# Performance work log

Measured on AMD Instinct MI355X. Metric: run time of the kernel, lower is better.

Reference implementation:

```python
import itertools
import jax, jax.numpy as jnp
import numpy as np

B, RES, RES_, STRIDE = 512, 14, 7, 2
IN_DIM, OUT_DIM, KEY_DIM, H, ATTN_RATIO = 256, 512, 16, 8, 2
NH_KD = KEY_DIM * H          # 128
D = ATTN_RATIO * KEY_DIM     # 32
DH = D * H                   # 256
KV_OUT = DH + NH_KD          # 384
N, N_ = RES * RES, RES_ * RES_   # 196, 49
EPS = 1e-5
SCALE = KEY_DIM ** -0.5


def _build_bias_idxs():
    points = list(itertools.product(range(RES), range(RES)))
    points_ = list(itertools.product(range(RES_), range(RES_)))
    offsets, idxs = {}, []
    for p1 in points_:
        for p2 in points:
            off = (abs(p1[0] * STRIDE - p2[0]), abs(p1[1] * STRIDE - p2[1]))
            if off not in offsets:
                offsets[off] = len(offsets)
            idxs.append(offsets[off])
    return np.array(idxs, dtype=np.int32).reshape(N_, N), len(offsets)


def _bn(x, g, b, m, v):
    # inference-mode BatchNorm1d over last dim
    return (x - m) * (g * jax.lax.rsqrt(v + EPS)) + b


def _hardswish(x):
    return x * jnp.clip(x + 3.0, 0.0, 6.0) * (1.0 / 6.0)


def setup_inputs() -> dict:
    key = jax.random.key(0)
    ks = jax.random.split(key, 16)
    idxs_np, n_off = _build_bias_idxs()
    inp = {
        "x": jax.random.normal(ks[0], (B, N, IN_DIM), jnp.float32),
        "w_kv": jax.random.normal(ks[1], (KV_OUT, IN_DIM), jnp.float32) * 0.02,
        "kv_g": jnp.ones((KV_OUT,), jnp.float32),
        "kv_b": jax.random.normal(ks[2], (KV_OUT,), jnp.float32) * 0.01,
        "kv_m": jax.random.normal(ks[3], (KV_OUT,), jnp.float32) * 0.01,
        "kv_v": jax.random.uniform(ks[4], (KV_OUT,), jnp.float32) + 0.5,
        "w_q": jax.random.normal(ks[5], (NH_KD, IN_DIM), jnp.float32) * 0.02,
        "q_g": jnp.ones((NH_KD,), jnp.float32),
        "q_b": jax.random.normal(ks[6], (NH_KD,), jnp.float32) * 0.01,
        "q_m": jax.random.normal(ks[7], (NH_KD,), jnp.float32) * 0.01,
        "q_v": jax.random.uniform(ks[8], (NH_KD,), jnp.float32) + 0.5,
        "w_p": jax.random.normal(ks[9], (OUT_DIM, DH), jnp.float32) * 0.02,
        "p_g": jnp.ones((OUT_DIM,), jnp.float32),
        "p_b": jax.random.normal(ks[10], (OUT_DIM,), jnp.float32) * 0.01,
        "p_m": jax.random.normal(ks[11], (OUT_DIM,), jnp.float32) * 0.01,
        "p_v": jax.random.uniform(ks[12], (OUT_DIM,), jnp.float32) + 0.5,
        "ab_table": jax.random.normal(ks[13], (H, n_off), jnp.float32) * 0.02,
        "bias_idxs": jnp.asarray(idxs_np),  # [N_, N] int32
    }
    return inp


def reference(x, w_kv, kv_g, kv_b, kv_m, kv_v,
              w_q, q_g, q_b, q_m, q_v,
              w_p, p_g, p_b, p_m, p_v,
              ab_table, bias_idxs):
    Bx = x.shape[0]
    # kv projection: [B, N, KV_OUT] -> split heads into k [B,H,N,KEY_DIM], v [B,H,N,D]
    kv = _bn(jnp.einsum('bnc,oc->bno', x, w_kv), kv_g, kv_b, kv_m, kv_v)
    kv = kv.reshape(Bx, N, H, KEY_DIM + D)
    k = kv[..., :KEY_DIM].transpose(0, 2, 1, 3)   # [B,H,N,KEY_DIM]
    v = kv[..., KEY_DIM:].transpose(0, 2, 1, 3)   # [B,H,N,D]
    # query path: spatial subsample then Linear+BN
    xs = x.reshape(Bx, RES, RES, IN_DIM)[:, ::STRIDE, ::STRIDE].reshape(Bx, N_, IN_DIM)
    q = _bn(jnp.einsum('bnc,oc->bno', xs, w_q), q_g, q_b, q_m, q_v)
    q = q.reshape(Bx, N_, H, KEY_DIM).transpose(0, 2, 1, 3)  # [B,H,N_,KEY_DIM]
    # relative-position bias gather: [H, N_, N]
    ab = ab_table[:, bias_idxs]
    attn = jnp.einsum('bhqd,bhkd->bhqk', q, k) * SCALE + ab
    attn = jax.nn.softmax(attn, axis=-1)
    out = jnp.einsum('bhqk,bhkd->bhqd', attn, v)           # [B,H,N_,D]
    out = out.transpose(0, 2, 1, 3).reshape(Bx, N_, DH)
    out = _hardswish(out)
    out = _bn(jnp.einsum('bnd,od->bno', out, w_p), p_g, p_b, p_m, p_v)
    return out
```

## Files before the change

### kernel.cpp

```cpp
#include <hip/hip_runtime.h>

typedef __attribute__((ext_vector_type(8))) short bf16x8;
typedef __attribute__((ext_vector_type(4))) float f32x4;
typedef __attribute__((ext_vector_type(4))) short short4v;
typedef __attribute__((ext_vector_type(4))) unsigned int u32x4;
typedef __attribute__((ext_vector_type(2))) unsigned int u32x2;

#define DEVFN static __device__ __forceinline__

DEVFN short f2bf(float f) {
  unsigned int u = __builtin_bit_cast(unsigned int, f);
  unsigned int r = (u + 0x7FFFu + ((u >> 16) & 1u)) >> 16;
  return (short)r;
}

DEVFN unsigned int pack2bf(float a, float b) {
  unsigned int lo = (unsigned int)(unsigned short)f2bf(a);
  unsigned int hi = (unsigned int)(unsigned short)f2bf(b);
  return lo | (hi << 16);
}

DEVFN f32x4 mfma_bf16(bf16x8 a, bf16x8 b, f32x4 c) {
  return __builtin_amdgcn_mfma_f32_16x16x32_bf16(a, b, c, 0, 0, 0);
}

DEVFN f32x4 zero4() { f32x4 z = {0.f, 0.f, 0.f, 0.f}; return z; }
DEVFN bf16x8 zero8() { bf16x8 z = {0,0,0,0,0,0,0,0}; return z; }

DEVFN void gload_lds16(const void* g, void* l) {
  __builtin_amdgcn_global_load_lds(
      (const __attribute__((address_space(1))) unsigned int*)g,
      (__attribute__((address_space(3))) unsigned int*)l, 16, 0, 0);
}

DEVFN bf16x8 lds8(const short* p) {
  short4v lo = *reinterpret_cast<const short4v*>(p);
  short4v hi = *reinterpret_cast<const short4v*>(p + 4);
  bf16x8 r;
  r[0] = lo[0]; r[1] = lo[1]; r[2] = lo[2]; r[3] = lo[3];
  r[4] = hi[0]; r[5] = hi[1]; r[6] = hi[2]; r[7] = hi[3];
  return r;
}

DEVFN bf16x8 cvt8v(float4 u0, float4 u1) {
  bf16x8 r;
  r[0] = f2bf(u0.x); r[1] = f2bf(u0.y); r[2] = f2bf(u0.z); r[3] = f2bf(u0.w);
  r[4] = f2bf(u1.x); r[5] = f2bf(u1.y); r[6] = f2bf(u1.z); r[7] = f2bf(u1.w);
  return r;
}

DEVFN float bfhi2f(unsigned int hi16) {
  return __builtin_bit_cast(float, hi16 << 16);
}
DEVFN float bfhi2f_hi(unsigned int word) {
  return __builtin_bit_cast(float, word & 0xffff0000u);
}

__global__ void pack_w_k(const float* __restrict__ w, const float* __restrict__ g,
                         const float* __restrict__ b, const float* __restrict__ m,
                         const float* __restrict__ v, short* __restrict__ pk,
                         float* __restrict__ bias, int O) {
  const int t = blockIdx.x * 256 + threadIdx.x;
  const int nt = O >> 4;
  const int total = nt * 8 * 64;
  if (t < total) {
    int lane = t & 63;
    int j = (t >> 6) % nt;
    int c = (t >> 6) / nt;
    int row = j * 16 + (lane & 15);
    int col = c * 32 + (lane >> 4) * 8;
    float s = g[row] * rsqrtf(v[row] + 1e-5f);
    const float* wp = w + (size_t)row * 256 + col;
    short* o = pk + (size_t)t * 8;
#pragma unroll
    for (int e = 0; e < 8; ++e) o[e] = f2bf(wp[e] * s);
  }
  if (t < O) {
    float s = g[t] * rsqrtf(v[t] + 1e-5f);
    bias[t] = b[t] - m[t] * s;
  }
}

__global__ void ab_gather2(const float* __restrict__ tab,
                           const int* __restrict__ idxs,
                           u32x2* __restrict__ ab3, int n_off) {
  const int blk = blockIdx.x;
  const int t = blk % 13, w = (blk / 13) & 3, h = blk / 52;
  const int lane = threadIdx.x;
  const int l15 = lane & 15, g = lane >> 4;
  int q = w * 16 + l15; if (q > 48) q = 48;
  const int nb = (t >> 1) * 32 + g * 8 + (t & 1) * 4;
  u32x2 out; out[0] = 0u; out[1] = 0u;
  if (nb < 196) {
    const int* irow = idxs + q * 196 + nb;
    const float* th = tab + h * n_off;
    out[0] = pack2bf(th[irow[0]], th[irow[1]]);
    out[1] = pack2bf(th[irow[2]], th[irow[3]]);
  }
  ab3[(size_t)blk * 64 + lane] = out;
}

__global__ __launch_bounds__(512, 4) void kv_gemm5(
    const float* __restrict__ x, const short* __restrict__ pk,
    const float* __restrict__ bias, short* __restrict__ k_out,
    short* __restrict__ vT_out) {
  __shared__ short xs2[16384];
  const int tid = threadIdx.x, w = tid >> 6, lane = tid & 63;
  const int l15 = lane & 15, g = lane >> 4;
  const int mt = blockIdx.x;

  const float* xb = x + (size_t)mt * 64 * 256;
#pragma unroll
  for (int it = 0; it < 4; ++it) {
    int i = it * 512 + tid;
    int row = i >> 5, gc = i & 31;
    const float* src = xb + row * 256 + gc * 8;
    float4 u0 = *reinterpret_cast<const float4*>(src);
    float4 u1 = *reinterpret_cast<const float4*>(src + 4);
    *reinterpret_cast<bf16x8*>(reinterpret_cast<char*>(xs2) + row * 512 +
                               ((gc * 16) ^ ((row & 7) << 4))) = cvt8v(u0, u1);
  }
  __syncthreads();

  f32x4 acc[4][3];
#pragma unroll
  for (int m = 0; m < 4; ++m) {
    acc[m][0] = zero4(); acc[m][1] = zero4(); acc[m][2] = zero4();
  }
  const int swz = (l15 & 7) << 4;
#pragma unroll
  for (int c = 0; c < 8; ++c) {
    bf16x8 wf0 = *reinterpret_cast<const bf16x8*>(pk + ((size_t)(c * 24 + 3 * w) * 64 + lane) * 8);
    bf16x8 wf1 = *reinterpret_cast<const bf16x8*>(pk + ((size_t)(c * 24 + 3 * w + 1) * 64 + lane) * 8);
    bf16x8 wf2 = *reinterpret_cast<const bf16x8*>(pk + ((size_t)(c * 24 + 3 * w + 2) * 64 + lane) * 8);
#pragma unroll
    for (int m = 0; m < 4; ++m) {
      const int row = m * 16 + l15;
      bf16x8 a = *reinterpret_cast<const bf16x8*>(
          reinterpret_cast<const char*>(xs2) + row * 512 +
          ((c * 64 + g * 16) ^ swz));
      acc[m][0] = mfma_bf16(a, wf0, acc[m][0]);
      acc[m][1] = mfma_bf16(a, wf1, acc[m][1]);
      acc[m][2] = mfma_bf16(a, wf2, acc[m][2]);
    }
  }

  const float bvK = bias[(3 * w) * 16 + l15];
  const float bv1 = bias[(3 * w + 1) * 16 + l15];
  const float bv2 = bias[(3 * w + 2) * 16 + l15];
#pragma unroll
  for (int m = 0; m < 4; ++m) {
    const int row0 = mt * 64 + m * 16 + g * 4;
    const int bb_ = row0 / 196, n0 = row0 % 196;
    short* kp = k_out + ((size_t)(bb_ * 8 + w) * 196 + n0) * 16 + l15;
#pragma unroll
    for (int r = 0; r < 4; ++r) kp[r * 16] = f2bf(acc[m][0][r] + bvK);
    short4v sv;
#pragma unroll
    for (int r = 0; r < 4; ++r) sv[r] = f2bf(acc[m][1][r] + bv1);
    *reinterpret_cast<short4v*>(
        vT_out + ((size_t)(bb_ * 8 + w) * 32 + l15) * 196 + n0) = sv;
#pragma unroll
    for (int r = 0; r < 4; ++r) sv[r] = f2bf(acc[m][2][r] + bv2);
    *reinterpret_cast<short4v*>(
        vT_out + ((size_t)(bb_ * 8 + w) * 32 + 16 + l15) * 196 + n0) = sv;
  }
}

__global__ __launch_bounds__(256) void q_gemm2(
    const float* __restrict__ x, const short* __restrict__ pk,
    const float* __restrict__ bias, short* __restrict__ out) {
  __shared__ short bs[8 * 512];
  __shared__ float sb[128];
  const int tid = threadIdx.x, w_id = tid >> 6, lane = tid & 63;
  const int l15 = lane & 15, gq = lane >> 4;
  const int mt = blockIdx.x;
  if (tid < 128) sb[tid] = bias[tid];
  const int arow = mt * 64 + w_id * 16 + l15;
  const int b = arow / 49, qi = arow % 49;
  const int n = 28 * (qi / 7) + 2 * (qi % 7);
  const float* xrow = x + ((size_t)b * 196 + n) * 256;

  f32x4 acc[8];
#pragma unroll
  for (int j = 0; j < 8; ++j) acc[j] = zero4();

  for (int c = 0; c < 8; ++c) {
    for (int seg = w_id; seg < 8; seg += 4)
      gload_lds16(pk + ((size_t)(c * 8 + seg) * 64 + lane) * 8, &bs[seg * 512]);
    const float4 u0 = *reinterpret_cast<const float4*>(xrow + c * 32 + gq * 8);
    const float4 u1 = *reinterpret_cast<const float4*>(xrow + c * 32 + gq * 8 + 4);
    bf16x8 a = cvt8v(u0, u1);
    __syncthreads();
#pragma unroll
    for (int j = 0; j < 8; ++j) {
      bf16x8 bj = *reinterpret_cast<const bf16x8*>(&bs[(j * 64 + lane) * 8]);
      acc[j] = mfma_bf16(a, bj, acc[j]);
    }
    __syncthreads();
  }
  const int orow = mt * 64 + w_id * 16 + gq * 4;
#pragma unroll
  for (int j = 0; j < 8; ++j) {
    int ch = j * 16 + l15;
    float bb = sb[ch];
#pragma unroll
    for (int r = 0; r < 4; ++r)
      out[(size_t)(orow + r) * 128 + ch] = f2bf(acc[j][r] + bb);
  }
}

__global__ __launch_bounds__(256) void attn4_k(
    const short* __restrict__ k_ws, const short* __restrict__ vT_ws,
    const short* __restrict__ qw, const u32x2* __restrict__ ab3,
    short* __restrict__ out) {
  __shared__ short vt[6304];
  __shared__ short kst[3200];
  const int b = blockIdx.x >> 3, h = blockIdx.x & 7;
  const int tid = threadIdx.x, w_id = tid >> 6, lane = tid & 63;
  const int l15 = lane & 15, g = lane >> 4;

  if (tid < 16) *reinterpret_cast<unsigned int*>(&vt[6272 + tid * 2]) = 0u;

  const short* vsrc = vT_ws + (size_t)(b * 8 + h) * 6272;
  for (int s = w_id; s < 13; s += 4) {
    if (s * 64 + lane < 784)
      gload_lds16(vsrc + (size_t)(s * 64 + lane) * 8, &vt[s * 512]);
  }
  const short* ksrc = k_ws + (size_t)(b * 8 + h) * 3136;
  for (int s = w_id; s < 7; s += 4) {
    if (s * 64 + lane < 392)
      gload_lds16(ksrc + (size_t)(s * 64 + lane) * 8, &kst[s * 512]);
  }

  const int q = w_id * 16 + l15;
  const bool qok = q < 49;
  bf16x8 bq = zero8();
  if (g < 2 && qok)
    bq = *reinterpret_cast<const bf16x8*>(
        qw + ((size_t)b * 49 + q) * 128 + h * 16 + g * 8);

  __syncthreads();

  f32x4 s[13];
#pragma unroll
  for (int t = 0; t < 13; ++t) {
    int n_a = (t >> 1) * 32 + (l15 >> 2) * 8 + (t & 1) * 4 + (l15 & 3);
    bf16x8 ak = zero8();
    if (g < 2 && n_a < 196) ak = lds8(&kst[n_a * 16 + g * 8]);
    s[t] = mfma_bf16(ak, bq, zero4());
  }

  const u32x2* abp = ab3 + (size_t)((h * 4 + w_id) * 13) * 64 + lane;
#pragma unroll
  for (int t = 0; t < 13; ++t) {
    int nb = (t >> 1) * 32 + g * 8 + (t & 1) * 4;
    if (nb < 196) {
      u32x2 bv = abp[t * 64];
      s[t][0] = s[t][0] * 0.25f + bfhi2f(bv[0]);
      s[t][1] = s[t][1] * 0.25f + bfhi2f_hi(bv[0]);
      s[t][2] = s[t][2] * 0.25f + bfhi2f(bv[1]);
      s[t][3] = s[t][3] * 0.25f + bfhi2f_hi(bv[1]);
    } else {
      s[t][0] = -1e30f; s[t][1] = -1e30f; s[t][2] = -1e30f; s[t][3] = -1e30f;
    }
  }

  float mx = s[0][0];
#pragma unroll
  for (int t = 0; t < 13; ++t)
    mx = fmaxf(mx, fmaxf(fmaxf(s[t][0], s[t][1]), fmaxf(s[t][2], s[t][3])));
  mx = fmaxf(mx, __shfl_xor(mx, 16, 64));
  mx = fmaxf(mx, __shfl_xor(mx, 32, 64));
  float sum = 0.f;
#pragma unroll
  for (int t = 0; t < 13; ++t) {
#pragma unroll
    for (int r = 0; r < 4; ++r) {
      float e = __expf(s[t][r] - mx);
      s[t][r] = e;
      sum += e;
    }
  }
  sum += __shfl_xor(sum, 16, 64);
  sum += __shfl_xor(sum, 32, 64);
  const float inv = 1.f / sum;

  unsigned int pkr[14][2];
#pragma unroll
  for (int t = 0; t < 13; ++t) {
    pkr[t][0] = pack2bf(s[t][0] * inv, s[t][1] * inv);
    pkr[t][1] = pack2bf(s[t][2] * inv, s[t][3] * inv);
  }
  pkr[13][0] = 0u; pkr[13][1] = 0u;

  f32x4 o0 = zero4(), o1 = zero4();
#pragma unroll
  for (int c = 0; c < 7; ++c) {
    u32x4 bp_u;
    bp_u[0] = pkr[2 * c][0];     bp_u[1] = pkr[2 * c][1];
    bp_u[2] = pkr[2 * c + 1][0]; bp_u[3] = pkr[2 * c + 1][1];
    bf16x8 bp = __builtin_bit_cast(bf16x8, bp_u);
    bf16x8 a0 = lds8(&vt[l15 * 196 + c * 32 + g * 8]);
    bf16x8 a1 = lds8(&vt[(16 + l15) * 196 + c * 32 + g * 8]);
    o0 = mfma_bf16(a0, bp, o0);
    o1 = mfma_bf16(a1, bp, o1);
  }

  if (qok) {
    short* op = out + (((size_t)b * 49 + q) * 256 + h * 32 + g * 4);
    short4v v0, v1;
#pragma unroll
    for (int r = 0; r < 4; ++r) {
      float x0 = o0[r];
      v0[r] = f2bf(x0 * fminf(fmaxf(x0 + 3.f, 0.f), 6.f) * (1.f / 6.f));
      float x1 = o1[r];
      v1[r] = f2bf(x1 * fminf(fmaxf(x1 + 3.f, 0.f), 6.f) * (1.f / 6.f));
    }
    *reinterpret_cast<short4v*>(op) = v0;
    *reinterpret_cast<short4v*>(op + 16) = v1;
  }
}

__global__ void p_gemm3(
    const short* __restrict__ a_in, const short* __restrict__ pk,
    const float* __restrict__ bias, float* __restrict__ out) {
  __shared__ short as_[32 * 256];
  const int tid = threadIdx.x, w = tid >> 6, lane = tid & 63;
  const int l15 = lane & 15, g = lane >> 4;
  const int half = blockIdx.x & 1;
  const int mt = blockIdx.x >> 1;

  const short* ab_ = a_in + (size_t)mt * 32 * 256;
#pragma unroll
  for (int it = 0; it < 4; ++it) {
    int i = it * 256 + tid;
    int row = i >> 5, gc = i & 31;
    bf16x8 vv = *reinterpret_cast<const bf16x8*>(ab_ + row * 256 + gc * 8);
    *reinterpret_cast<bf16x8*>(reinterpret_cast<char*>(as_) + row * 512 +
                               ((gc * 16) ^ ((row & 7) << 4))) = vv;
  }
  __syncthreads();

  f32x4 acc[2][4];
#pragma unroll
  for (int m = 0; m < 2; ++m)
#pragma unroll
    for (int jj = 0; jj < 4; ++jj) acc[m][jj] = zero4();

  const int jbase = half * 16 + w * 4;
#pragma unroll
  for (int c = 0; c < 8; ++c) {
    bf16x8 wf[4];
#pragma unroll
    for (int jj = 0; jj < 4; ++jj)
      wf[jj] = *reinterpret_cast<const bf16x8*>(
          pk + ((size_t)(c * 32 + jbase + jj) * 64 + lane) * 8);
#pragma unroll
    for (int m = 0; m < 2; ++m) {
      const int row = m * 16 + l15;
      bf16x8 a = *reinterpret_cast<const bf16x8*>(
          reinterpret_cast<const char*>(as_) + row * 512 +
          ((c * 64 + g * 16) ^ ((row & 7) << 4)));
#pragma unroll
      for (int jj = 0; jj < 4; ++jj)
        acc[m][jj] = mfma_bf16(a, wf[jj], acc[m][jj]);
    }
  }

#pragma unroll
  for (int m = 0; m < 2; ++m) {
    const int row0 = mt * 32 + m * 16 + g * 4;
#pragma unroll
    for (int jj = 0; jj < 4; ++jj) {
      const int och = (jbase + jj) * 16 + l15;
      const float bv = bias[och];
#pragma unroll
      for (int r = 0; r < 4; ++r)
        out[(size_t)(row0 + r) * 512 + och] = acc[m][jj][r] + bv;
    }
  }
}

extern "C" void kernel_launch(void* const* d_in, const int* in_sizes, int n_in,
                              void* d_out, int out_size, void* d_ws, size_t ws_size,
                              hipStream_t stream) {
  const float* x    = (const float*)d_in[0];
  const float* w_kv = (const float*)d_in[1];
  const float* kv_g = (const float*)d_in[2];
  const float* kv_b = (const float*)d_in[3];
  const float* kv_m = (const float*)d_in[4];
  const float* kv_v = (const float*)d_in[5];
  const float* w_q  = (const float*)d_in[6];
  const float* q_g  = (const float*)d_in[7];
  const float* q_b  = (const float*)d_in[8];
  const float* q_m  = (const float*)d_in[9];
  const float* q_v  = (const float*)d_in[10];
  const float* w_p  = (const float*)d_in[11];
  const float* p_g  = (const float*)d_in[12];
  const float* p_b  = (const float*)d_in[13];
  const float* p_m  = (const float*)d_in[14];
  const float* p_v  = (const float*)d_in[15];
  const float* ab_t = (const float*)d_in[16];
  const int*   idxs = (const int*)d_in[17];
  const int n_off = in_sizes[16] / 8;

  char* ws = (char*)d_ws;
  short* pk_kv  = (short*)(ws);
  short* pk_q   = (short*)(ws + 196608);
  short* pk_p   = (short*)(ws + 262144);
  float* bs_kv  = (float*)(ws + 524288);
  float* bs_q   = (float*)(ws + 525824);
  float* bs_p   = (float*)(ws + 526336);
  u32x2* ab3_ws = (u32x2*)(ws + 528384);
  short* k_ws   = (short*)(ws + 835712);
  short* vT_ws  = (short*)(ws + 26525824);
  short* q_ws   = (short*)(ws + 77906048);
  short* at_ws  = (short*)(ws + 84328576);

  pack_w_k<<<dim3(48), dim3(256), 0, stream>>>(w_kv, kv_g, kv_b, kv_m, kv_v, pk_kv, bs_kv, 384);
  pack_w_k<<<dim3(16), dim3(256), 0, stream>>>(w_q, q_g, q_b, q_m, q_v, pk_q, bs_q, 128);
  pack_w_k<<<dim3(64), dim3(256), 0, stream>>>(w_p, p_g, p_b, p_m, p_v, pk_p, bs_p, 512);
  ab_gather2<<<dim3(416), dim3(64), 0, stream>>>(ab_t, idxs, ab3_ws, n_off);

  kv_gemm5<<<dim3(1568), dim3(512), 0, stream>>>(x, pk_kv, bs_kv, k_ws, vT_ws);
  q_gemm2<<<dim3(392), dim3(256), 0, stream>>>(x, pk_q, bs_q, q_ws);
  attn4_k<<<dim3(4096), dim3(256), 0, stream>>>(k_ws, vT_ws, q_ws, ab3_ws, at_ws);
  p_gemm3<<<dim3(1568), dim3(256), 0, stream>>>(at_ws, pk_p, bs_p, (float*)d_out);
}
```

Measured before the change: 128.5 us.

## Fuse KV projection into attention kernel and prepack x into MFMA bf16 tiles

```diff
diff --git a/kernel.cpp b/kernel.cpp
--- a/kernel.cpp
+++ b/kernel.cpp
@@ -81,6 +81,21 @@
   }
 }
 
+__global__ __launch_bounds__(512) void pack_x2(const float* __restrict__ x,
+                                               short* __restrict__ xP) {
+  const int bt = blockIdx.x;
+  const int tile = bt % 13, b = bt / 13;
+  const int tid = threadIdx.x;
+  const int c = tid >> 6, lane = tid & 63;
+  const int l15 = lane & 15, g = lane >> 4;
+  int row = tile * 16 + l15; if (row > 195) row = 195;
+  const float* src = x + ((size_t)b * 196 + row) * 256 + c * 32 + g * 8;
+  float4 u0 = *reinterpret_cast<const float4*>(src);
+  float4 u1 = *reinterpret_cast<const float4*>(src + 4);
+  *reinterpret_cast<bf16x8*>(xP + (((size_t)bt * 8 + c) * 64 + lane) * 8) =
+      cvt8v(u0, u1);
+}
+
 __global__ void ab_gather2(const float* __restrict__ tab,
                            const int* __restrict__ idxs,
                            u32x2* __restrict__ ab3, int n_off) {
@@ -100,73 +115,6 @@
   ab3[(size_t)blk * 64 + lane] = out;
 }
 
-__global__ __launch_bounds__(512, 4) void kv_gemm5(
-    const float* __restrict__ x, const short* __restrict__ pk,
-    const float* __restrict__ bias, short* __restrict__ k_out,
-    short* __restrict__ vT_out) {
-  __shared__ short xs2[16384];
-  const int tid = threadIdx.x, w = tid >> 6, lane = tid & 63;
-  const int l15 = lane & 15, g = lane >> 4;
-  const int mt = blockIdx.x;
-
-  const float* xb = x + (size_t)mt * 64 * 256;
-#pragma unroll
-  for (int it = 0; it < 4; ++it) {
-    int i = it * 512 + tid;
-    int row = i >> 5, gc = i & 31;
-    const float* src = xb + row * 256 + gc * 8;
-    float4 u0 = *reinterpret_cast<const float4*>(src);
-    float4 u1 = *reinterpret_cast<const float4*>(src + 4);
-    *reinterpret_cast<bf16x8*>(reinterpret_cast<char*>(xs2) + row * 512 +
-                               ((gc * 16) ^ ((row & 7) << 4))) = cvt8v(u0, u1);
-  }
-  __syncthreads();
-
-  f32x4 acc[4][3];
-#pragma unroll
-  for (int m = 0; m < 4; ++m) {
-    acc[m][0] = zero4(); acc[m][1] = zero4(); acc[m][2] = zero4();
-  }
-  const int swz = (l15 & 7) << 4;
-#pragma unroll
-  for (int c = 0; c < 8; ++c) {
-    bf16x8 wf0 = *reinterpret_cast<const bf16x8*>(pk + ((size_t)(c * 24 + 3 * w) * 64 + lane) * 8);
-    bf16x8 wf1 = *reinterpret_cast<const bf16x8*>(pk + ((size_t)(c * 24 + 3 * w + 1) * 64 + lane) * 8);
-    bf16x8 wf2 = *reinterpret_cast<const bf16x8*>(pk + ((size_t)(c * 24 + 3 * w + 2) * 64 + lane) * 8);
-#pragma unroll
-    for (int m = 0; m < 4; ++m) {
-      const int row = m * 16 + l15;
-      bf16x8 a = *reinterpret_cast<const bf16x8*>(
-          reinterpret_cast<const char*>(xs2) + row * 512 +
-          ((c * 64 + g * 16) ^ swz));
-      acc[m][0] = mfma_bf16(a, wf0, acc[m][0]);
-      acc[m][1] = mfma_bf16(a, wf1, acc[m][1]);
-      acc[m][2] = mfma_bf16(a, wf2, acc[m][2]);
-    }
-  }
-
-  const float bvK = bias[(3 * w) * 16 + l15];
-  const float bv1 = bias[(3 * w + 1) * 16 + l15];
-  const float bv2 = bias[(3 * w + 2) * 16 + l15];
-#pragma unroll
-  for (int m = 0; m < 4; ++m) {
-    const int row0 = mt * 64 + m * 16 + g * 4;
-    const int bb_ = row0 / 196, n0 = row0 % 196;
-    short* kp = k_out + ((size_t)(bb_ * 8 + w) * 196 + n0) * 16 + l15;
-#pragma unroll
-    for (int r = 0; r < 4; ++r) kp[r * 16] = f2bf(acc[m][0][r] + bvK);
-    short4v sv;
-#pragma unroll
-    for (int r = 0; r < 4; ++r) sv[r] = f2bf(acc[m][1][r] + bv1);
-    *reinterpret_cast<short4v*>(
-        vT_out + ((size_t)(bb_ * 8 + w) * 32 + l15) * 196 + n0) = sv;
-#pragma unroll
-    for (int r = 0; r < 4; ++r) sv[r] = f2bf(acc[m][2][r] + bv2);
-    *reinterpret_cast<short4v*>(
-        vT_out + ((size_t)(bb_ * 8 + w) * 32 + 16 + l15) * 196 + n0) = sv;
-  }
-}
-
 __global__ __launch_bounds__(256) void q_gemm2(
     const float* __restrict__ x, const short* __restrict__ pk,
     const float* __restrict__ bias, short* __restrict__ out) {
@@ -210,115 +158,167 @@
   }
 }
 
-__global__ __launch_bounds__(256) void attn4_k(
-    const short* __restrict__ k_ws, const short* __restrict__ vT_ws,
+__global__ __launch_bounds__(256) void attn5_k(
+    const short* __restrict__ xP,
+    const short* __restrict__ pkv, const float* __restrict__ bkv,
     const short* __restrict__ qw, const u32x2* __restrict__ ab3,
     short* __restrict__ out) {
-  __shared__ short vt[6304];
-  __shared__ short kst[3200];
-  const int b = blockIdx.x >> 3, h = blockIdx.x & 7;
-  const int tid = threadIdx.x, w_id = tid >> 6, lane = tid & 63;
+  __shared__ short ks[3200];
+  __shared__ short vs[6304];
+  const int j = blockIdx.x;
+  const int b = (j % 8) + 8 * (j / 32);
+  const int h0 = ((j / 8) % 4) * 2;
+  const int tid = threadIdx.x, w = tid >> 6, lane = tid & 63;
   const int l15 = lane & 15, g = lane >> 4;
 
-  if (tid < 16) *reinterpret_cast<unsigned int*>(&vt[6272 + tid * 2]) = 0u;
-
-  const short* vsrc = vT_ws + (size_t)(b * 8 + h) * 6272;
-  for (int s = w_id; s < 13; s += 4) {
-    if (s * 64 + lane < 784)
-      gload_lds16(vsrc + (size_t)(s * 64 + lane) * 8, &vt[s * 512]);
-  }
-  const short* ksrc = k_ws + (size_t)(b * 8 + h) * 3136;
-  for (int s = w_id; s < 7; s += 4) {
-    if (s * 64 + lane < 392)
-      gload_lds16(ksrc + (size_t)(s * 64 + lane) * 8, &kst[s * 512]);
-  }
-
-  const int q = w_id * 16 + l15;
+  if (tid < 16) *reinterpret_cast<unsigned int*>(&vs[6272 + tid * 2]) = 0u;
+
+  const int q = w * 16 + l15;
   const bool qok = q < 49;
-  bf16x8 bq = zero8();
-  if (g < 2 && qok)
-    bq = *reinterpret_cast<const bf16x8*>(
-        qw + ((size_t)b * 49 + q) * 128 + h * 16 + g * 8);
-
-  __syncthreads();
-
-  f32x4 s[13];
-#pragma unroll
-  for (int t = 0; t < 13; ++t) {
-    int n_a = (t >> 1) * 32 + (l15 >> 2) * 8 + (t & 1) * 4 + (l15 & 3);
-    bf16x8 ak = zero8();
-    if (g < 2 && n_a < 196) ak = lds8(&kst[n_a * 16 + g * 8]);
-    s[t] = mfma_bf16(ak, bq, zero4());
-  }
-
-  const u32x2* abp = ab3 + (size_t)((h * 4 + w_id) * 13) * 64 + lane;
-#pragma unroll
-  for (int t = 0; t < 13; ++t) {
-    int nb = (t >> 1) * 32 + g * 8 + (t & 1) * 4;
-    if (nb < 196) {
-      u32x2 bv = abp[t * 64];
-      s[t][0] = s[t][0] * 0.25f + bfhi2f(bv[0]);
-      s[t][1] = s[t][1] * 0.25f + bfhi2f_hi(bv[0]);
-      s[t][2] = s[t][2] * 0.25f + bfhi2f(bv[1]);
-      s[t][3] = s[t][3] * 0.25f + bfhi2f_hi(bv[1]);
-    } else {
-      s[t][0] = -1e30f; s[t][1] = -1e30f; s[t][2] = -1e30f; s[t][3] = -1e30f;
+  const short* xPb = xP + (size_t)b * 13 * 8 * 512;
+
+#pragma unroll 1
+  for (int hh = 0; hh < 2; ++hh) {
+    const int h = h0 + hh;
+
+    {
+      f32x4 aK[4], a0[4], a1[4];
+#pragma unroll
+      for (int ti = 0; ti < 4; ++ti) {
+        aK[ti] = zero4(); a0[ti] = zero4(); a1[ti] = zero4();
+      }
+#pragma unroll
+      for (int c = 0; c < 8; ++c) {
+        bf16x8 wf0 = *reinterpret_cast<const bf16x8*>(
+            pkv + ((size_t)(c * 24 + 3 * h) * 64 + lane) * 8);
+        bf16x8 wf1 = *reinterpret_cast<const bf16x8*>(
+            pkv + ((size_t)(c * 24 + 3 * h + 1) * 64 + lane) * 8);
+        bf16x8 wf2 = *reinterpret_cast<const bf16x8*>(
+            pkv + ((size_t)(c * 24 + 3 * h + 2) * 64 + lane) * 8);
+#pragma unroll
+        for (int ti = 0; ti < 4; ++ti) {
+          const int tile = w + ti * 4;
+          if (tile < 13) {
+            bf16x8 a = *reinterpret_cast<const bf16x8*>(
+                xPb + (((size_t)tile * 8 + c) * 64 + lane) * 8);
+            aK[ti] = mfma_bf16(a, wf0, aK[ti]);
+            a0[ti] = mfma_bf16(wf1, a, a0[ti]);
+            a1[ti] = mfma_bf16(wf2, a, a1[ti]);
+          }
+        }
+      }
+      const float  bvK = bkv[3 * h * 16 + l15];
+      const float4 bv0 = *reinterpret_cast<const float4*>(bkv + (3 * h + 1) * 16 + g * 4);
+      const float4 bv1 = *reinterpret_cast<const float4*>(bkv + (3 * h + 2) * 16 + g * 4);
+#pragma unroll
+      for (int ti = 0; ti < 4; ++ti) {
+        const int tile = w + ti * 4;
+        if (tile < 13) {
+#pragma unroll
+          for (int r = 0; r < 4; ++r) {
+            int n = tile * 16 + g * 4 + r;
+            if (n < 196) ks[n * 16 + l15] = f2bf(aK[ti][r] + bvK);
+          }
+          int nv = tile * 16 + l15;
+          if (nv < 196) {
+#pragma unroll
+            for (int r = 0; r < 4; ++r)
+              vs[(g * 4 + r) * 196 + nv] = f2bf(a0[ti][r] + bv0[r]);
+#pragma unroll
+            for (int r = 0; r < 4; ++r)
+              vs[(16 + g * 4 + r) * 196 + nv] = f2bf(a1[ti][r] + bv1[r]);
+          }
+        }
+      }
     }
-  }
-
-  float mx = s[0][0];
-#pragma unroll
-  for (int t = 0; t < 13; ++t)
-    mx = fmaxf(mx, fmaxf(fmaxf(s[t][0], s[t][1]), fmaxf(s[t][2], s[t][3])));
-  mx = fmaxf(mx, __shfl_xor(mx, 16, 64));
-  mx = fmaxf(mx, __shfl_xor(mx, 32, 64));
-  float sum = 0.f;
-#pragma unroll
-  for (int t = 0; t < 13; ++t) {
-#pragma unroll
-    for (int r = 0; r < 4; ++r) {
-      float e = __expf(s[t][r] - mx);
-      s[t][r] = e;
-      sum += e;
+    __syncthreads();
+
+    {
+      bf16x8 bq = zero8();
+      if (g < 2 && qok)
+        bq = *reinterpret_cast<const bf16x8*>(
+            qw + ((size_t)b * 49 + q) * 128 + h * 16 + g * 8);
+
+      f32x4 s[13];
+#pragma unroll
+      for (int t = 0; t < 13; ++t) {
+        int n_a = (t >> 1) * 32 + (l15 >> 2) * 8 + (t & 1) * 4 + (l15 & 3);
+        bf16x8 ak = zero8();
+        if (g < 2 && n_a < 196) ak = lds8(&ks[n_a * 16 + g * 8]);
+        s[t] = mfma_bf16(ak, bq, zero4());
+      }
+
+      const u32x2* abp = ab3 + (size_t)((h * 4 + w) * 13) * 64 + lane;
+#pragma unroll
+      for (int t = 0; t < 13; ++t) {
+        int nb = (t >> 1) * 32 + g * 8 + (t & 1) * 4;
+        if (nb < 196) {
+          u32x2 bv = abp[t * 64];
+          s[t][0] = s[t][0] * 0.25f + bfhi2f(bv[0]);
+          s[t][1] = s[t][1] * 0.25f + bfhi2f_hi(bv[0]);
+          s[t][2] = s[t][2] * 0.25f + bfhi2f(bv[1]);
+          s[t][3] = s[t][3] * 0.25f + bfhi2f_hi(bv[1]);
+        } else {
+          s[t][0] = -1e30f; s[t][1] = -1e30f; s[t][2] = -1e30f; s[t][3] = -1e30f;
+        }
+      }
+
+      float mx = s[0][0];
+#pragma unroll
+      for (int t = 0; t < 13; ++t)
+        mx = fmaxf(mx, fmaxf(fmaxf(s[t][0], s[t][1]), fmaxf(s[t][2], s[t][3])));
+      mx = fmaxf(mx, __shfl_xor(mx, 16, 64));
+      mx = fmaxf(mx, __shfl_xor(mx, 32, 64));
+      float sum = 0.f;
+#pragma unroll
+      for (int t = 0; t < 13; ++t) {
+#pragma unroll
+        for (int r = 0; r < 4; ++r) {
+          float e = __expf(s[t][r] - mx);
+          s[t][r] = e;
+          sum += e;
+        }
+      }
+      sum += __shfl_xor(sum, 16, 64);
+      sum += __shfl_xor(sum, 32, 64);
+      const float inv = 1.f / sum;
+
+      unsigned int pkr[14][2];
+#pragma unroll
+      for (int t = 0; t < 13; ++t) {
+        pkr[t][0] = pack2bf(s[t][0] * inv, s[t][1] * inv);
+        pkr[t][1] = pack2bf(s[t][2] * inv, s[t][3] * inv);
+      }
+      pkr[13][0] = 0u; pkr[13][1] = 0u;
+
+      f32x4 o0 = zero4(), o1 = zero4();
+#pragma unroll
+      for (int c = 0; c < 7; ++c) {
+        u32x4 bp_u;
+        bp_u[0] = pkr[2 * c][0];     bp_u[1] = pkr[2 * c][1];
+        bp_u[2] = pkr[2 * c + 1][0]; bp_u[3] = pkr[2 * c + 1][1];
+        bf16x8 bp = __builtin_bit_cast(bf16x8, bp_u);
+        bf16x8 va0 = lds8(&vs[l15 * 196 + c * 32 + g * 8]);
+        bf16x8 va1 = lds8(&vs[(16 + l15) * 196 + c * 32 + g * 8]);
+        o0 = mfma_bf16(va0, bp, o0);
+        o1 = mfma_bf16(va1, bp, o1);
+      }
+
+      if (qok) {
+        short* op = out + (((size_t)b * 49 + q) * 256 + h * 32 + g * 4);
+        short4v v0, v1;
+#pragma unroll
+        for (int r = 0; r < 4; ++r) {
+          float x0 = o0[r];
+          v0[r] = f2bf(x0 * fminf(fmaxf(x0 + 3.f, 0.f), 6.f) * (1.f / 6.f));
+          float x1 = o1[r];
+          v1[r] = f2bf(x1 * fminf(fmaxf(x1 + 3.f, 0.f), 6.f) * (1.f / 6.f));
+        }
+        *reinterpret_cast<short4v*>(op) = v0;
+        *reinterpret_cast<short4v*>(op + 16) = v1;
+      }
     }
-  }
-  sum += __shfl_xor(sum, 16, 64);
-  sum += __shfl_xor(sum, 32, 64);
-  const float inv = 1.f / sum;
-
-  unsigned int pkr[14][2];
-#pragma unroll
-  for (int t = 0; t < 13; ++t) {
-    pkr[t][0] = pack2bf(s[t][0] * inv, s[t][1] * inv);
-    pkr[t][1] = pack2bf(s[t][2] * inv, s[t][3] * inv);
-  }
-  pkr[13][0] = 0u; pkr[13][1] = 0u;
-
-  f32x4 o0 = zero4(), o1 = zero4();
-#pragma unroll
-  for (int c = 0; c < 7; ++c) {
-    u32x4 bp_u;
-    bp_u[0] = pkr[2 * c][0];     bp_u[1] = pkr[2 * c][1];
-    bp_u[2] = pkr[2 * c + 1][0]; bp_u[3] = pkr[2 * c + 1][1];
-    bf16x8 bp = __builtin_bit_cast(bf16x8, bp_u);
-    bf16x8 a0 = lds8(&vt[l15 * 196 + c * 32 + g * 8]);
-    bf16x8 a1 = lds8(&vt[(16 + l15) * 196 + c * 32 + g * 8]);
-    o0 = mfma_bf16(a0, bp, o0);
-    o1 = mfma_bf16(a1, bp, o1);
-  }
-
-  if (qok) {
-    short* op = out + (((size_t)b * 49 + q) * 256 + h * 32 + g * 4);
-    short4v v0, v1;
-#pragma unroll
-    for (int r = 0; r < 4; ++r) {
-      float x0 = o0[r];
-      v0[r] = f2bf(x0 * fminf(fmaxf(x0 + 3.f, 0.f), 6.f) * (1.f / 6.f));
-      float x1 = o1[r];
-      v1[r] = f2bf(x1 * fminf(fmaxf(x1 + 3.f, 0.f), 6.f) * (1.f / 6.f));
-    }
-    *reinterpret_cast<short4v*>(op) = v0;
-    *reinterpret_cast<short4v*>(op + 16) = v1;
+    __syncthreads();
   }
 }
 
@@ -413,18 +413,17 @@
   float* bs_q   = (float*)(ws + 525824);
   float* bs_p   = (float*)(ws + 526336);
   u32x2* ab3_ws = (u32x2*)(ws + 528384);
-  short* k_ws   = (short*)(ws + 835712);
-  short* vT_ws  = (short*)(ws + 26525824);
-  short* q_ws   = (short*)(ws + 77906048);
-  short* at_ws  = (short*)(ws + 84328576);
+  short* xP_ws  = (short*)(ws + 835712);
+  short* q_ws   = (short*)(ws + 55361664);
+  short* at_ws  = (short*)(ws + 61784192);
 
   pack_w_k<<<dim3(48), dim3(256), 0, stream>>>(w_kv, kv_g, kv_b, kv_m, kv_v, pk_kv, bs_kv, 384);
   pack_w_k<<<dim3(16), dim3(256), 0, stream>>>(w_q, q_g, q_b, q_m, q_v, pk_q, bs_q, 128);
   pack_w_k<<<dim3(64), dim3(256), 0, stream>>>(w_p, p_g, p_b, p_m, p_v, pk_p, bs_p, 512);
   ab_gather2<<<dim3(416), dim3(64), 0, stream>>>(ab_t, idxs, ab3_ws, n_off);
-
-  kv_gemm5<<<dim3(1568), dim3(512), 0, stream>>>(x, pk_kv, bs_kv, k_ws, vT_ws);
+  pack_x2<<<dim3(6656), dim3(512), 0, stream>>>(x, xP_ws);
+
   q_gemm2<<<dim3(392), dim3(256), 0, stream>>>(x, pk_q, bs_q, q_ws);
-  attn4_k<<<dim3(4096), dim3(256), 0, stream>>>(k_ws, vT_ws, q_ws, ab3_ws, at_ws);
+  attn5_k<<<dim3(2048), dim3(256), 0, stream>>>(xP_ws, pk_kv, bs_kv, q_ws, ab3_ws, at_ws);
   p_gemm3<<<dim3(1568), dim3(256), 0, stream>>>(at_ws, pk_p, bs_p, (float*)d_out);
 }
```

Result: slower. 331.6 us (+158.0%).
